# Kernel tuning notes

Hardware: AMD Instinct MI355X
Metric: run time of the kernel (lower is better)

The kernel has to match this reference:

```python
import jax, jax.numpy as jnp
import numpy as np


def setup_inputs() -> dict:
    key = jax.random.key(0)
    k1, k2, k3 = jax.random.split(key, 3)
    M, C, N, K, L = 4, 2, 512, 16000, 16
    mixture_w = jax.random.normal(k1, (M, N, K), dtype=jnp.float32)
    est_mask = jax.random.uniform(k2, (M, C, N, K), dtype=jnp.float32)
    W = jax.random.normal(k3, (L, N), dtype=jnp.float32) * (1.0 / np.sqrt(N))
    return {"mixture_w": mixture_w, "est_mask": est_mask, "W": W}


def reference(mixture_w, est_mask, W):
    # mixture_w: [M, N, K]; est_mask: [M, C, N, K]; W: [L, N] (torch Linear weight)
    L = W.shape[0]
    hop = L // 2
    source_w = mixture_w[:, None] * est_mask            # [M, C, N, K]
    frames = jnp.einsum('mcnk,ln->mckl', source_w, W)   # [M, C, K, L]
    M, C, K, Lf = frames.shape
    T = (K - 1) * hop + Lf
    # overlap-and-add: frame k writes to samples [k*hop, k*hop+L)
    idx = (jnp.arange(K)[:, None] * hop + jnp.arange(Lf)[None, :]).reshape(-1)
    est_source = jnp.zeros((M, C, T), frames.dtype).at[:, :, idx].add(
        frames.reshape(M, C, K * Lf))
    return est_source
```

## Files before the change

kernel.cpp:

```cpp
#include <hip/hip_runtime.h>


#define M_   4
#define C_   2
#define N_   512
#define K_   16000
#define L_   16
#define HOP  8
#define T_   ((K_ - 1) * HOP + L_)
#define BK   64
#define NSEG 4
#define NPW  (N_ / NSEG)
#define NCH  (NPW / 4)
#define NB   (K_ / BK)
#define NUNITS (M_ * NB)
#define GRID (NUNITS * C_)
#define RSTRIDE 20
#define WS_TAIL_OFF (M_ * C_ * NB * 8)

__global__ __launch_bounds__(256, 8)
void decoder_kernel(const float* __restrict__ mix,
                    const float* __restrict__ mask,
                    const float* __restrict__ Wg,
                    float* __restrict__ out,
                    float* __restrict__ ws) {
    __shared__ float lds[3 * 64 * RSTRIDE];

    const int tid  = threadIdx.x;
    const int lane = tid & 63;
    const int w    = tid >> 6;
    const int bidx = blockIdx.x;
    const int c    = (bidx >> 3) & 1;
    const int unit = ((bidx >> 4) << 3) | (bidx & 7);
    const int m    = unit / NB;
    const int bb   = unit % NB;
    const int k0   = bb * BK;

    float acc[16];
    #pragma unroll
    for (int i = 0; i < 16; ++i) acc[i] = 0.f;

    const int n0w  = w * NPW;
    const int n0wU = __builtin_amdgcn_readfirstlane(n0w);
    const int kk   = k0 + lane;
    const float* pm = mix  + (size_t)m * N_ * K_ + (size_t)n0w * K_ + kk;
    const float* pk = mask + ((size_t)(m * C_ + c) * N_ + n0w) * K_ + kk;

    #pragma unroll 2
    for (int ch = 0; ch < NCH; ++ch) {
        float mv[4], av[4];
        #pragma unroll
        for (int j = 0; j < 4; ++j) {
            mv[j] = pm[(size_t)j * K_];
            av[j] = pk[(size_t)j * K_];
        }
        float s[4];
        #pragma unroll
        for (int j = 0; j < 4; ++j) s[j] = mv[j] * av[j];

        const int nbase = n0wU + ch * 4;
        #pragma unroll
        for (int l = 0; l < L_; ++l) {
            const float4 w4 = *(const float4*)&Wg[l * N_ + nbase];
            acc[l] = fmaf(s[0], w4.x, acc[l]);
            acc[l] = fmaf(s[1], w4.y, acc[l]);
            acc[l] = fmaf(s[2], w4.z, acc[l]);
            acc[l] = fmaf(s[3], w4.w, acc[l]);
        }
        pm += (size_t)4 * K_;
        pk += (size_t)4 * K_;
    }

    __syncthreads();
    if (w > 0) {
        float* rb = &lds[(w - 1) * (64 * RSTRIDE) + lane * RSTRIDE];
        #pragma unroll
        for (int i = 0; i < 4; ++i)
            *(float4*)&rb[i * 4] = make_float4(acc[i*4], acc[i*4+1],
                                               acc[i*4+2], acc[i*4+3]);
    }
    __syncthreads();

    if (w == 0) {
        #pragma unroll
        for (int r = 0; r < 3; ++r) {
            const float* rb = &lds[r * (64 * RSTRIDE) + lane * RSTRIDE];
            #pragma unroll
            for (int i = 0; i < 4; ++i) {
                const float4 v = *(const float4*)&rb[i * 4];
                acc[i*4]   += v.x;  acc[i*4+1] += v.y;
                acc[i*4+2] += v.z;  acc[i*4+3] += v.w;
            }
        }

        float* ob = out + (size_t)(m * C_ + c) * T_ + (size_t)kk * HOP;
        float cmb[8];
        #pragma unroll
        for (int j = 0; j < 8; ++j) {
            const float pv = __shfl_up(acc[8 + j], 1);
            cmb[j] = acc[j] + pv;
        }
        if (lane == 0) {
            float* hb = ws + (size_t)((m * C_ + c) * NB + bb) * 8;
            *(float4*)&hb[0] = make_float4(acc[0], acc[1], acc[2], acc[3]);
            *(float4*)&hb[4] = make_float4(acc[4], acc[5], acc[6], acc[7]);
        } else {
            *(float4*)&ob[0] = make_float4(cmb[0], cmb[1], cmb[2], cmb[3]);
            *(float4*)&ob[4] = make_float4(cmb[4], cmb[5], cmb[6], cmb[7]);
        }
        if (lane == 63) {
            float* tb = ws + WS_TAIL_OFF + (size_t)((m * C_ + c) * NB + bb) * 8;
            *(float4*)&tb[0] = make_float4(acc[8],  acc[9],  acc[10], acc[11]);
            *(float4*)&tb[4] = make_float4(acc[12], acc[13], acc[14], acc[15]);
        }
    }
}

__global__ __launch_bounds__(256)
void boundary_kernel(const float* __restrict__ ws, float* __restrict__ out) {
    const int id = blockIdx.x * 256 + threadIdx.x;
    const int total = M_ * C_ * NB * 8;
    if (id >= total) return;
    const int j  = id & 7;
    const int bb = (id >> 3) % NB;
    const int mc = (id >> 3) / NB;
    float v = ws[(size_t)(mc * NB + bb) * 8 + j];
    if (bb > 0) v += ws[WS_TAIL_OFF + (size_t)(mc * NB + bb - 1) * 8 + j];
    out[(size_t)mc * T_ + (size_t)bb * (BK * HOP) + j] = v;
    if (bb == NB - 1) {
        out[(size_t)mc * T_ + (size_t)K_ * HOP + j] =
            ws[WS_TAIL_OFF + (size_t)(mc * NB + bb) * 8 + j];
    }
}

extern "C" void kernel_launch(void* const* d_in, const int* in_sizes, int n_in,
                              void* d_out, int out_size, void* d_ws, size_t ws_size,
                              hipStream_t stream) {
    const float* mix  = (const float*)d_in[0];
    const float* mask = (const float*)d_in[1];
    const float* Wg   = (const float*)d_in[2];
    float* out = (float*)d_out;
    float* ws  = (float*)d_ws;

    decoder_kernel<<<dim3(GRID), dim3(256), 0, stream>>>(mix, mask, Wg, out, ws);
    boundary_kernel<<<dim3((M_ * C_ * NB * 8 + 255) / 256), dim3(256), 0, stream>>>(ws, out);
}
```

Measured before the change: 80.78 us.

## Process both mask channels per block to reuse mixture loads

Result: slower. 105.4 us (+30.4%).

```diff
diff --git a/kernel.cpp b/kernel.cpp
--- a/kernel.cpp
+++ b/kernel.cpp
@@ -11,10 +11,9 @@
 #define BK   64
 #define NSEG 4
 #define NPW  (N_ / NSEG)
-#define NCH  (NPW / 4)
+#define NCH  (NPW / 2)
 #define NB   (K_ / BK)
-#define NUNITS (M_ * NB)
-#define GRID (NUNITS * C_)
+#define GRID (M_ * NB)
 #define RSTRIDE 20
 #define WS_TAIL_OFF (M_ * C_ * NB * 8)
 
@@ -29,90 +28,101 @@
     const int tid  = threadIdx.x;
     const int lane = tid & 63;
     const int w    = tid >> 6;
-    const int bidx = blockIdx.x;
-    const int c    = (bidx >> 3) & 1;
-    const int unit = ((bidx >> 4) << 3) | (bidx & 7);
-    const int m    = unit / NB;
-    const int bb   = unit % NB;
+    const int m    = blockIdx.x / NB;
+    const int bb   = blockIdx.x % NB;
     const int k0   = bb * BK;
 
-    float acc[16];
+    float acc0[16], acc1[16];
     #pragma unroll
-    for (int i = 0; i < 16; ++i) acc[i] = 0.f;
+    for (int i = 0; i < 16; ++i) { acc0[i] = 0.f; acc1[i] = 0.f; }
 
     const int n0w  = w * NPW;
     const int n0wU = __builtin_amdgcn_readfirstlane(n0w);
     const int kk   = k0 + lane;
-    const float* pm = mix  + (size_t)m * N_ * K_ + (size_t)n0w * K_ + kk;
-    const float* pk = mask + ((size_t)(m * C_ + c) * N_ + n0w) * K_ + kk;
+
+    const float* mixB = mix  + (size_t)m * N_ * K_ + (size_t)n0w * K_;
+    const float* m0B  = mask + ((size_t)(m * C_) * N_ + n0w) * K_;
+    const float* m1B  = m0B + (size_t)N_ * K_;
+    int off = kk;
 
     #pragma unroll 2
     for (int ch = 0; ch < NCH; ++ch) {
-        float mv[4], av[4];
-        #pragma unroll
-        for (int j = 0; j < 4; ++j) {
-            mv[j] = pm[(size_t)j * K_];
-            av[j] = pk[(size_t)j * K_];
-        }
-        float s[4];
-        #pragma unroll
-        for (int j = 0; j < 4; ++j) s[j] = mv[j] * av[j];
+        const int o0 = off, o1 = off + K_;
+        const float mv0 = mixB[o0], mv1 = mixB[o1];
+        const float a00 = m0B[o0],  a01 = m0B[o1];
+        const float a10 = m1B[o0],  a11 = m1B[o1];
+        const float s00 = mv0 * a00, s01 = mv1 * a01;
+        const float s10 = mv0 * a10, s11 = mv1 * a11;
 
-        const int nbase = n0wU + ch * 4;
+        const int nbase = n0wU + ch * 2;
         #pragma unroll
         for (int l = 0; l < L_; ++l) {
-            const float4 w4 = *(const float4*)&Wg[l * N_ + nbase];
-            acc[l] = fmaf(s[0], w4.x, acc[l]);
-            acc[l] = fmaf(s[1], w4.y, acc[l]);
-            acc[l] = fmaf(s[2], w4.z, acc[l]);
-            acc[l] = fmaf(s[3], w4.w, acc[l]);
+            const float2 w2 = *(const float2*)&Wg[l * N_ + nbase];
+            acc0[l] = fmaf(s00, w2.x, acc0[l]);
+            acc0[l] = fmaf(s01, w2.y, acc0[l]);
+            acc1[l] = fmaf(s10, w2.x, acc1[l]);
+            acc1[l] = fmaf(s11, w2.y, acc1[l]);
         }
-        pm += (size_t)4 * K_;
-        pk += (size_t)4 * K_;
+        off += 2 * K_;
     }
 
-    __syncthreads();
-    if (w > 0) {
-        float* rb = &lds[(w - 1) * (64 * RSTRIDE) + lane * RSTRIDE];
-        #pragma unroll
-        for (int i = 0; i < 4; ++i)
-            *(float4*)&rb[i * 4] = make_float4(acc[i*4], acc[i*4+1],
-                                               acc[i*4+2], acc[i*4+3]);
-    }
-    __syncthreads();
+    auto reduce_c = [&](float (&acc)[16]) {
+        __syncthreads();
+        if (w > 0) {
+            float* rb = &lds[(w - 1) * (64 * RSTRIDE) + lane * RSTRIDE];
+            #pragma unroll
+            for (int i = 0; i < 4; ++i)
+                *(float4*)&rb[i * 4] = make_float4(acc[i*4], acc[i*4+1],
+                                                   acc[i*4+2], acc[i*4+3]);
+        }
+        __syncthreads();
+        if (w == 0) {
+            #pragma unroll
+            for (int r = 0; r < 3; ++r) {
+                const float* rb = &lds[r * (64 * RSTRIDE) + lane * RSTRIDE];
+                #pragma unroll
+                for (int i = 0; i < 4; ++i) {
+                    const float4 v = *(const float4*)&rb[i * 4];
+                    acc[i*4]   += v.x;  acc[i*4+1] += v.y;
+                    acc[i*4+2] += v.z;  acc[i*4+3] += v.w;
+                }
+            }
+        }
+    };
+    reduce_c(acc0);
+    reduce_c(acc1);
 
     if (w == 0) {
-        #pragma unroll
-        for (int r = 0; r < 3; ++r) {
-            const float* rb = &lds[r * (64 * RSTRIDE) + lane * RSTRIDE];
-            #pragma unroll
-            for (int i = 0; i < 4; ++i) {
-                const float4 v = *(const float4*)&rb[i * 4];
-                acc[i*4]   += v.x;  acc[i*4+1] += v.y;
-                acc[i*4+2] += v.z;  acc[i*4+3] += v.w;
-            }
+#define EPILOGUE(ACC, CIDX)                                                   \
+        {                                                                     \
+            float* ob = out + (size_t)(m * C_ + (CIDX)) * T_                  \
+                            + (size_t)kk * HOP;                               \
+            float cmb[8];                                                     \
+            _Pragma("unroll")                                                 \
+            for (int j = 0; j < 8; ++j) {                                     \
+                const float pv = __shfl_up(ACC[8 + j], 1);                    \
+                cmb[j] = ACC[j] + pv;                                         \
+            }                                                                 \
+            if (lane == 0) {                                                  \
+                float* hb = ws + (size_t)((m * C_ + (CIDX)) * NB + bb) * 8;   \
+                *(float4*)&hb[0] = make_float4(ACC[0], ACC[1], ACC[2], ACC[3]);\
+                *(float4*)&hb[4] = make_float4(ACC[4], ACC[5], ACC[6], ACC[7]);\
+            } else {                                                          \
+                *(float4*)&ob[0] = make_float4(cmb[0], cmb[1], cmb[2], cmb[3]);\
+                *(float4*)&ob[4] = make_float4(cmb[4], cmb[5], cmb[6], cmb[7]);\
+            }                                                                 \
+            if (lane == 63) {                                                 \
+                float* tb = ws + WS_TAIL_OFF                                  \
+                             + (size_t)((m * C_ + (CIDX)) * NB + bb) * 8;     \
+                *(float4*)&tb[0] = make_float4(ACC[8],  ACC[9],               \
+                                               ACC[10], ACC[11]);             \
+                *(float4*)&tb[4] = make_float4(ACC[12], ACC[13],              \
+                                               ACC[14], ACC[15]);             \
+            }                                                                 \
         }
-
-        float* ob = out + (size_t)(m * C_ + c) * T_ + (size_t)kk * HOP;
-        float cmb[8];
-        #pragma unroll
-        for (int j = 0; j < 8; ++j) {
-            const float pv = __shfl_up(acc[8 + j], 1);
-            cmb[j] = acc[j] + pv;
-        }
-        if (lane == 0) {
-            float* hb = ws + (size_t)((m * C_ + c) * NB + bb) * 8;
-            *(float4*)&hb[0] = make_float4(acc[0], acc[1], acc[2], acc[3]);
-            *(float4*)&hb[4] = make_float4(acc[4], acc[5], acc[6], acc[7]);
-        } else {
-            *(float4*)&ob[0] = make_float4(cmb[0], cmb[1], cmb[2], cmb[3]);
-            *(float4*)&ob[4] = make_float4(cmb[4], cmb[5], cmb[6], cmb[7]);
-        }
-        if (lane == 63) {
-            float* tb = ws + WS_TAIL_OFF + (size_t)((m * C_ + c) * NB + bb) * 8;
-            *(float4*)&tb[0] = make_float4(acc[8],  acc[9],  acc[10], acc[11]);
-            *(float4*)&tb[4] = make_float4(acc[12], acc[13], acc[14], acc[15]);
-        }
+        EPILOGUE(acc0, 0)
+        EPILOGUE(acc1, 1)
+#undef EPILOGUE
     }
 }
 
```

## Share mixture loads across both sources via LDS staging in merged blocks

Applied to the files above, without the earlier changes.

Measured after the change: 81.11 us. About the same (+0.4%).

```diff
diff --git a/kernel.cpp b/kernel.cpp
--- a/kernel.cpp
+++ b/kernel.cpp
@@ -9,71 +9,84 @@
 #define HOP  8
 #define T_   ((K_ - 1) * HOP + L_)
 #define BK   64
-#define NSEG 4
-#define NPW  (N_ / NSEG)
-#define NCH  (NPW / 4)
 #define NB   (K_ / BK)
-#define NUNITS (M_ * NB)
-#define GRID (NUNITS * C_)
+#define GRID (M_ * NB)
+#define NPW  128
+#define SG   8
+#define NSTEP (NPW / SG)
 #define RSTRIDE 20
 #define WS_TAIL_OFF (M_ * C_ * NB * 8)
 
-__global__ __launch_bounds__(256, 8)
+__global__ __launch_bounds__(512, 8)
 void decoder_kernel(const float* __restrict__ mix,
                     const float* __restrict__ mask,
                     const float* __restrict__ Wg,
                     float* __restrict__ out,
                     float* __restrict__ ws) {
-    __shared__ float lds[3 * 64 * RSTRIDE];
+    __shared__ float lds[7680];
 
     const int tid  = threadIdx.x;
     const int lane = tid & 63;
     const int w    = tid >> 6;
-    const int bidx = blockIdx.x;
-    const int c    = (bidx >> 3) & 1;
-    const int unit = ((bidx >> 4) << 3) | (bidx & 7);
-    const int m    = unit / NB;
-    const int bb   = unit % NB;
+    const int c    = w >> 2;
+    const int g    = w & 3;
+    const int m    = blockIdx.x / NB;
+    const int bb   = blockIdx.x % NB;
     const int k0   = bb * BK;
+    const int kk   = k0 + lane;
 
     float acc[16];
     #pragma unroll
     for (int i = 0; i < 16; ++i) acc[i] = 0.f;
 
-    const int n0w  = w * NPW;
+    const int n0w  = g * NPW;
     const int n0wU = __builtin_amdgcn_readfirstlane(n0w);
-    const int kk   = k0 + lane;
-    const float* pm = mix  + (size_t)m * N_ * K_ + (size_t)n0w * K_ + kk;
-    const float* pk = mask + ((size_t)(m * C_ + c) * N_ + n0w) * K_ + kk;
 
-    #pragma unroll 2
-    for (int ch = 0; ch < NCH; ++ch) {
-        float mv[4], av[4];
+    const float* pmix = mix  + (size_t)m * N_ * K_ + (size_t)n0w * K_ + kk;
+    const float* pmsk = mask + ((size_t)(m * C_ + c) * N_ + n0w) * K_ + kk;
+
+    float* stg = &lds[(g * SG) * 64];
+
+    #pragma unroll 1
+    for (int st = 0; st < NSTEP; ++st) {
+        float mr[4];
         #pragma unroll
-        for (int j = 0; j < 4; ++j) {
-            mv[j] = pm[(size_t)j * K_];
-            av[j] = pk[(size_t)j * K_];
+        for (int i = 0; i < 4; ++i)
+            mr[i] = pmix[(size_t)(st * SG + c * 4 + i) * K_];
+        float a[8];
+        #pragma unroll
+        for (int j = 0; j < 8; ++j)
+            a[j] = pmsk[(size_t)(st * SG + j) * K_];
+
+        __syncthreads();
+        #pragma unroll
+        for (int i = 0; i < 4; ++i)
+            stg[(c * 4 + i) * 64 + lane] = mr[i];
+        __syncthreads();
+
+        #pragma unroll
+        for (int chh = 0; chh < 2; ++chh) {
+            float s[4];
+            #pragma unroll
+            for (int j = 0; j < 4; ++j) {
+                const float mv = stg[(chh * 4 + j) * 64 + lane];
+                s[j] = mv * a[chh * 4 + j];
+            }
+            const int nbase = n0wU + st * SG + chh * 4;
+            #pragma unroll
+            for (int l = 0; l < L_; ++l) {
+                const float4 w4 = *(const float4*)&Wg[l * N_ + nbase];
+                acc[l] = fmaf(s[0], w4.x, acc[l]);
+                acc[l] = fmaf(s[1], w4.y, acc[l]);
+                acc[l] = fmaf(s[2], w4.z, acc[l]);
+                acc[l] = fmaf(s[3], w4.w, acc[l]);
+            }
         }
-        float s[4];
-        #pragma unroll
-        for (int j = 0; j < 4; ++j) s[j] = mv[j] * av[j];
-
-        const int nbase = n0wU + ch * 4;
-        #pragma unroll
-        for (int l = 0; l < L_; ++l) {
-            const float4 w4 = *(const float4*)&Wg[l * N_ + nbase];
-            acc[l] = fmaf(s[0], w4.x, acc[l]);
-            acc[l] = fmaf(s[1], w4.y, acc[l]);
-            acc[l] = fmaf(s[2], w4.z, acc[l]);
-            acc[l] = fmaf(s[3], w4.w, acc[l]);
-        }
-        pm += (size_t)4 * K_;
-        pk += (size_t)4 * K_;
     }
 
     __syncthreads();
-    if (w > 0) {
-        float* rb = &lds[(w - 1) * (64 * RSTRIDE) + lane * RSTRIDE];
+    if (g > 0) {
+        float* rb = &lds[((c * 3 + (g - 1)) * 64 + lane) * RSTRIDE];
         #pragma unroll
         for (int i = 0; i < 4; ++i)
             *(float4*)&rb[i * 4] = make_float4(acc[i*4], acc[i*4+1],
@@ -81,10 +94,10 @@
     }
     __syncthreads();
 
-    if (w == 0) {
+    if (g == 0) {
         #pragma unroll
         for (int r = 0; r < 3; ++r) {
-            const float* rb = &lds[r * (64 * RSTRIDE) + lane * RSTRIDE];
+            const float* rb = &lds[((c * 3 + r) * 64 + lane) * RSTRIDE];
             #pragma unroll
             for (int i = 0; i < 4; ++i) {
                 const float4 v = *(const float4*)&rb[i * 4];
@@ -142,6 +155,6 @@
     float* out = (float*)d_out;
     float* ws  = (float*)d_ws;
 
-    decoder_kernel<<<dim3(GRID), dim3(256), 0, stream>>>(mix, mask, Wg, out, ws);
+    decoder_kernel<<<dim3(GRID), dim3(512), 0, stream>>>(mix, mask, Wg, out, ws);
     boundary_kernel<<<dim3((M_ * C_ * NB * 8 + 255) / 256), dim3(256), 0, stream>>>(ws, out);
 }
```
